# Optimization experiments

Measured on AMD Instinct MI355X. Metric: run time of the kernel, lower is better.

The kernel has to match this reference:

```python
import jax, jax.numpy as jnp
import numpy as np

B, N = 16, 131072
C_MID, C_OUT = 128, 16


def setup_inputs() -> dict:
    key = jax.random.key(0)
    k1, k2, k3, k4 = jax.random.split(key, 4)
    # points in roughly [-0.5, 0.5] so cube indexing covers the grids
    x = jax.random.uniform(k1, (B, N, 3), dtype=jnp.float32) - 0.5
    W1 = jax.random.normal(k2, (C_MID, 3), dtype=jnp.float32) * 0.1
    b1 = jnp.zeros((C_MID,), jnp.float32)
    W2 = jax.random.normal(k3, (C_OUT, C_MID), dtype=jnp.float32) * 0.1
    b2 = jnp.zeros((C_OUT,), jnp.float32)
    # fixed per-batch permutations (deterministic stand-in for torch.randperm)
    perm = jnp.stack([jax.random.permutation(jax.random.fold_in(k4, i), N)
                      for i in range(B)]).astype(jnp.int32)
    return {"x": x, "W1": W1, "b1": b1, "W2": W2, "b2": b2, "perm": perm}


def point_to_cell(pts, feat, W, H, D):
    # pts float [B,N,3] already clamped to [0, dim-1]; cast like torch LongTensor
    idx = pts.astype(jnp.int32)
    flat = (idx[..., 0] * H + idx[..., 1]) * D + idx[..., 2]  # [B,N]
    Bb, Nn, C = feat.shape

    def scatter_one(fi, fe):
        grid = jnp.zeros((W * H * D, C), feat.dtype)
        return grid.at[fi].set(fe)

    cell = jax.vmap(scatter_one)(flat, feat)           # [B, WHD, C]
    return cell.transpose(0, 2, 1).reshape(Bb, C, W, H, D)


def reference(x, W1, b1, W2, b2, perm):
    # PointNetfeatLocal: 1x1 Conv1d stack == per-point MLP 3 -> 128 -> 16
    h = jnp.maximum(jnp.einsum('bnc,hc->bnh', x, W1) + b1, 0.0)
    feat = jnp.einsum('bnh,oh->bno', h, W2) + b2       # [B,N,16]
    # shuffle_points_feat: per-batch permutation gather
    xs = jnp.take_along_axis(x, perm[..., None], axis=1)
    fs = jnp.take_along_axis(feat, perm[..., None], axis=1)
    # batch_grid_pooling32 / 64
    cube32 = jnp.clip(xs * 32.0 + 16.5, 0.0, 31.0)
    cube64 = jnp.clip(xs * 64.0 + 32.5, 0.0, 63.0)
    feat_cell32 = point_to_cell(cube32, fs, 32, 32, 32)  # [B,16,32,32,32]
    feat_cell64 = point_to_cell(cube64, fs, 64, 64, 64)  # [B,16,64,64,64]
    return feat_cell32, feat_cell64
```

## Files before the change

kernel.cpp:

```cpp
#include <hip/hip_runtime.h>

namespace {
constexpr int kB = 16;
constexpr int kN = 131072;
constexpr int kNLog = 17;
constexpr int kCMid = 128;
constexpr int kCOut = 16;
constexpr int kCells32Log = 15;
constexpr int kCells64Log = 18;
constexpr int kCells32 = 1 << kCells32Log;
constexpr int kCells64 = 1 << kCells64Log;
constexpr long kOut32Elems = (long)kB * kCOut * kCells32;
}

template <bool STORE_FEAT>
__global__ __launch_bounds__(256) void fused_mlp_scatter(
    const float* __restrict__ x,
    const float* __restrict__ W1, const float* __restrict__ b1,
    const float* __restrict__ W2, const float* __restrict__ b2,
    const int* __restrict__ perm,
    unsigned int* __restrict__ win32, unsigned int* __restrict__ win64,
    float* __restrict__ feat)
{
    __shared__ float sW1[kCMid * 3];
    __shared__ float sb1[kCMid];
    __shared__ float sW2[kCOut * kCMid];
    __shared__ float sb2[kCOut];
    const int t = threadIdx.x;
    if (STORE_FEAT) {
        for (int idx = t; idx < kCMid * 3; idx += 256) sW1[idx] = W1[idx];
        for (int idx = t; idx < kCMid; idx += 256) sb1[idx] = b1[idx];
        for (int idx = t; idx < kCOut * kCMid; idx += 256) sW2[idx] = W2[idx];
        if (t < kCOut) sb2[t] = b2[t];
        __syncthreads();
    }

    const long gid = (long)blockIdx.x * 256 + t;
    const int b = (int)(gid >> kNLog);
    const int i = (int)(gid & (kN - 1));
    const int j = perm[gid];

    const float* xp = x + ((long)b * kN + j) * 3;
    const float x0 = xp[0], x1 = xp[1], x2 = xp[2];

    const int ix32 = (int)fminf(fmaxf(__fadd_rn(__fmul_rn(x0, 32.0f), 16.5f), 0.0f), 31.0f);
    const int iy32 = (int)fminf(fmaxf(__fadd_rn(__fmul_rn(x1, 32.0f), 16.5f), 0.0f), 31.0f);
    const int iz32 = (int)fminf(fmaxf(__fadd_rn(__fmul_rn(x2, 32.0f), 16.5f), 0.0f), 31.0f);
    const int cell32 = (ix32 * 32 + iy32) * 32 + iz32;
    const int ix64 = (int)fminf(fmaxf(__fadd_rn(__fmul_rn(x0, 64.0f), 32.5f), 0.0f), 63.0f);
    const int iy64 = (int)fminf(fmaxf(__fadd_rn(__fmul_rn(x1, 64.0f), 32.5f), 0.0f), 63.0f);
    const int iz64 = (int)fminf(fmaxf(__fadd_rn(__fmul_rn(x2, 64.0f), 32.5f), 0.0f), 63.0f);
    const int cell64 = (ix64 * 64 + iy64) * 64 + iz64;

    const unsigned int pri = (unsigned int)(i + 1);
    atomicMax(&win32[b * kCells32 + cell32], pri);
    atomicMax(&win64[b * kCells64 + cell64], pri);

    if (STORE_FEAT) {
        float acc[kCOut];
        #pragma unroll
        for (int c = 0; c < kCOut; ++c) acc[c] = sb2[c];
        #pragma unroll 4
        for (int k = 0; k < kCMid; ++k) {
            float h = sW1[k * 3 + 0] * x0 + sW1[k * 3 + 1] * x1 + sW1[k * 3 + 2] * x2 + sb1[k];
            h = fmaxf(h, 0.0f);
            #pragma unroll
            for (int c = 0; c < kCOut; ++c) acc[c] += sW2[c * kCMid + k] * h;
        }
        float4* fp = (float4*)(feat + gid * kCOut);
        fp[0] = make_float4(acc[0], acc[1], acc[2], acc[3]);
        fp[1] = make_float4(acc[4], acc[5], acc[6], acc[7]);
        fp[2] = make_float4(acc[8], acc[9], acc[10], acc[11]);
        fp[3] = make_float4(acc[12], acc[13], acc[14], acc[15]);
    }
}

template <int CLOG, bool RECOMPUTE>
__global__ __launch_bounds__(256) void gather_cells(
    const unsigned int* __restrict__ win,
    const float* __restrict__ feat,
    const int* __restrict__ perm,
    const float* __restrict__ x,
    const float* __restrict__ W1, const float* __restrict__ b1,
    const float* __restrict__ W2, const float* __restrict__ b2,
    float* __restrict__ out)
{
    constexpr int cells = 1 << CLOG;
    __shared__ float sW1[kCMid * 3];
    __shared__ float sb1[kCMid];
    __shared__ float sW2[kCOut * kCMid];
    __shared__ float sb2[kCOut];
    const int t = threadIdx.x;
    if (RECOMPUTE) {
        for (int idx = t; idx < kCMid * 3; idx += 256) sW1[idx] = W1[idx];
        for (int idx = t; idx < kCMid; idx += 256) sb1[idx] = b1[idx];
        for (int idx = t; idx < kCOut * kCMid; idx += 256) sW2[idx] = W2[idx];
        if (t < kCOut) sb2[t] = b2[t];
        __syncthreads();
    }

    const long gid = (long)blockIdx.x * 256 + t;
    const int b = (int)(gid >> CLOG);
    const int cell = (int)(gid & (cells - 1));
    const unsigned int w = win[gid];

    float v[kCOut];
    if (w == 0u) {
        #pragma unroll
        for (int c = 0; c < kCOut; ++c) v[c] = 0.0f;
    } else if (!RECOMPUTE) {
        const int i = (int)(w - 1u);
        const float4* fp = (const float4*)(feat + (((long)b << kNLog) + i) * kCOut);
        float4 f0 = fp[0], f1 = fp[1], f2 = fp[2], f3 = fp[3];
        v[0] = f0.x; v[1] = f0.y; v[2]  = f0.z; v[3]  = f0.w;
        v[4] = f1.x; v[5] = f1.y; v[6]  = f1.z; v[7]  = f1.w;
        v[8] = f2.x; v[9] = f2.y; v[10] = f2.z; v[11] = f2.w;
        v[12] = f3.x; v[13] = f3.y; v[14] = f3.z; v[15] = f3.w;
    } else {
        const int i = (int)(w - 1u);
        const int j = perm[((long)b << kNLog) + i];
        const float* xp = x + ((long)b * kN + j) * 3;
        const float x0 = xp[0], x1 = xp[1], x2 = xp[2];
        #pragma unroll
        for (int c = 0; c < kCOut; ++c) v[c] = sb2[c];
        #pragma unroll 4
        for (int k = 0; k < kCMid; ++k) {
            float h = sW1[k * 3 + 0] * x0 + sW1[k * 3 + 1] * x1 + sW1[k * 3 + 2] * x2 + sb1[k];
            h = fmaxf(h, 0.0f);
            #pragma unroll
            for (int c = 0; c < kCOut; ++c) v[c] += sW2[c * kCMid + k] * h;
        }
    }

    float* op = out + (((long)b * kCOut) << CLOG) + cell;
    #pragma unroll
    for (int c = 0; c < kCOut; ++c) op[(long)c << CLOG] = v[c];
}

extern "C" void kernel_launch(void* const* d_in, const int* in_sizes, int n_in,
                              void* d_out, int out_size, void* d_ws, size_t ws_size,
                              hipStream_t stream)
{
    const float* x  = (const float*)d_in[0];
    const float* W1 = (const float*)d_in[1];
    const float* b1 = (const float*)d_in[2];
    const float* W2 = (const float*)d_in[3];
    const float* b2 = (const float*)d_in[4];
    const int* perm = (const int*)d_in[5];

    float* out32 = (float*)d_out;
    float* out64 = out32 + kOut32Elems;

    unsigned int* win32 = (unsigned int*)d_ws;
    unsigned int* win64 = win32 + (size_t)kB * kCells32;
    const size_t winnerBytes = (size_t)kB * (kCells32 + kCells64) * sizeof(unsigned int);
    float* feat = (float*)((char*)d_ws + winnerBytes);
    const size_t featBytes = (size_t)kB * kN * kCOut * sizeof(float);
    const bool storeFeat = ws_size >= winnerBytes + featBytes;

    hipMemsetAsync(d_ws, 0, winnerBytes, stream);

    const int nPtsBlocks = (int)(((long)kB * kN) / 256);
    const int n32Blocks  = (int)(((long)kB * kCells32) / 256);
    const int n64Blocks  = (int)(((long)kB * kCells64) / 256);
    dim3 blk(256);

    if (storeFeat) {
        fused_mlp_scatter<true><<<nPtsBlocks, blk, 0, stream>>>(
            x, W1, b1, W2, b2, perm, win32, win64, feat);
        gather_cells<kCells32Log, false><<<n32Blocks, blk, 0, stream>>>(
            win32, feat, perm, x, W1, b1, W2, b2, out32);
        gather_cells<kCells64Log, false><<<n64Blocks, blk, 0, stream>>>(
            win64, feat, perm, x, W1, b1, W2, b2, out64);
    } else {
        fused_mlp_scatter<false><<<nPtsBlocks, blk, 0, stream>>>(
            x, W1, b1, W2, b2, perm, win32, win64, nullptr);
        gather_cells<kCells32Log, true><<<n32Blocks, blk, 0, stream>>>(
            win32, feat, perm, x, W1, b1, W2, b2, out32);
        gather_cells<kCells64Log, true><<<n64Blocks, blk, 0, stream>>>(
            win64, feat, perm, x, W1, b1, W2, b2, out64);
    }
}
```

Measured before the change: 331.3 us.

## Pre-pack MLP weights and compute four points per thread with uniform weight loads

A tiny pre-kernel packs W1 together with b1 into float4 rows and stores W2 transposed, so that each k step reads contiguous float4 weights with a wave-uniform index. This replaces the per-block shared-memory staging and the LDS reads that fed every FMA. The scatter kernel now handles four points per thread, so each weight load is shared across four points and more FMAs are available to overlap with the atomics. In exchange it adds one extra launch and holds more accumulators in registers. The MLP kernel also now always writes feat, even on the fallback path where the workspace may be too small to hold it.

```diff
diff --git a/kernel.cpp b/kernel.cpp
--- a/kernel.cpp
+++ b/kernel.cpp
@@ -11,67 +11,104 @@
 constexpr int kCells32 = 1 << kCells32Log;
 constexpr int kCells64 = 1 << kCells64Log;
 constexpr long kOut32Elems = (long)kB * kCOut * kCells32;
-}
-
-template <bool STORE_FEAT>
+constexpr int kP = 4;
+}
+
+__global__ __launch_bounds__(256) void pack_weights(
+    const float* __restrict__ W1, const float* __restrict__ b1,
+    const float* __restrict__ W2,
+    float* __restrict__ W1p, float* __restrict__ W2t)
+{
+    const int t = threadIdx.x;
+    for (int k = t; k < kCMid; k += 256) {
+        W1p[k * 4 + 0] = W1[k * 3 + 0];
+        W1p[k * 4 + 1] = W1[k * 3 + 1];
+        W1p[k * 4 + 2] = W1[k * 3 + 2];
+        W1p[k * 4 + 3] = b1[k];
+    }
+    for (int idx = t; idx < kCOut * kCMid; idx += 256) {
+        const int c = idx >> 7;
+        const int k = idx & 127;
+        W2t[k * kCOut + c] = W2[idx];
+    }
+}
+
 __global__ __launch_bounds__(256) void fused_mlp_scatter(
     const float* __restrict__ x,
-    const float* __restrict__ W1, const float* __restrict__ b1,
-    const float* __restrict__ W2, const float* __restrict__ b2,
     const int* __restrict__ perm,
+    const float* __restrict__ W1p, const float* __restrict__ W2t,
+    const float* __restrict__ b2,
     unsigned int* __restrict__ win32, unsigned int* __restrict__ win64,
     float* __restrict__ feat)
 {
-    __shared__ float sW1[kCMid * 3];
-    __shared__ float sb1[kCMid];
-    __shared__ float sW2[kCOut * kCMid];
-    __shared__ float sb2[kCOut];
     const int t = threadIdx.x;
-    if (STORE_FEAT) {
-        for (int idx = t; idx < kCMid * 3; idx += 256) sW1[idx] = W1[idx];
-        for (int idx = t; idx < kCMid; idx += 256) sb1[idx] = b1[idx];
-        for (int idx = t; idx < kCOut * kCMid; idx += 256) sW2[idx] = W2[idx];
-        if (t < kCOut) sb2[t] = b2[t];
-        __syncthreads();
-    }
-
-    const long gid = (long)blockIdx.x * 256 + t;
-    const int b = (int)(gid >> kNLog);
-    const int i = (int)(gid & (kN - 1));
-    const int j = perm[gid];
-
-    const float* xp = x + ((long)b * kN + j) * 3;
-    const float x0 = xp[0], x1 = xp[1], x2 = xp[2];
-
-    const int ix32 = (int)fminf(fmaxf(__fadd_rn(__fmul_rn(x0, 32.0f), 16.5f), 0.0f), 31.0f);
-    const int iy32 = (int)fminf(fmaxf(__fadd_rn(__fmul_rn(x1, 32.0f), 16.5f), 0.0f), 31.0f);
-    const int iz32 = (int)fminf(fmaxf(__fadd_rn(__fmul_rn(x2, 32.0f), 16.5f), 0.0f), 31.0f);
-    const int cell32 = (ix32 * 32 + iy32) * 32 + iz32;
-    const int ix64 = (int)fminf(fmaxf(__fadd_rn(__fmul_rn(x0, 64.0f), 32.5f), 0.0f), 63.0f);
-    const int iy64 = (int)fminf(fmaxf(__fadd_rn(__fmul_rn(x1, 64.0f), 32.5f), 0.0f), 63.0f);
-    const int iz64 = (int)fminf(fmaxf(__fadd_rn(__fmul_rn(x2, 64.0f), 32.5f), 0.0f), 63.0f);
-    const int cell64 = (ix64 * 64 + iy64) * 64 + iz64;
-
-    const unsigned int pri = (unsigned int)(i + 1);
-    atomicMax(&win32[b * kCells32 + cell32], pri);
-    atomicMax(&win64[b * kCells64 + cell64], pri);
-
-    if (STORE_FEAT) {
-        float acc[kCOut];
-        #pragma unroll
-        for (int c = 0; c < kCOut; ++c) acc[c] = sb2[c];
-        #pragma unroll 4
-        for (int k = 0; k < kCMid; ++k) {
-            float h = sW1[k * 3 + 0] * x0 + sW1[k * 3 + 1] * x1 + sW1[k * 3 + 2] * x2 + sb1[k];
-            h = fmaxf(h, 0.0f);
+    const long base = (long)blockIdx.x * (256 * kP);
+
+    float x0[kP], x1[kP], x2[kP];
+
+    #pragma unroll
+    for (int p = 0; p < kP; ++p) {
+        const long gid = base + p * 256 + t;
+        const int b = (int)(gid >> kNLog);
+        const int i = (int)(gid & (kN - 1));
+        const int j = perm[gid];
+        const float* xp = x + ((long)b * kN + j) * 3;
+        const float v0 = xp[0], v1 = xp[1], v2 = xp[2];
+        x0[p] = v0; x1[p] = v1; x2[p] = v2;
+
+        const int ix32 = (int)fminf(fmaxf(__fadd_rn(__fmul_rn(v0, 32.0f), 16.5f), 0.0f), 31.0f);
+        const int iy32 = (int)fminf(fmaxf(__fadd_rn(__fmul_rn(v1, 32.0f), 16.5f), 0.0f), 31.0f);
+        const int iz32 = (int)fminf(fmaxf(__fadd_rn(__fmul_rn(v2, 32.0f), 16.5f), 0.0f), 31.0f);
+        const int ix64 = (int)fminf(fmaxf(__fadd_rn(__fmul_rn(v0, 64.0f), 32.5f), 0.0f), 63.0f);
+        const int iy64 = (int)fminf(fmaxf(__fadd_rn(__fmul_rn(v1, 64.0f), 32.5f), 0.0f), 63.0f);
+        const int iz64 = (int)fminf(fmaxf(__fadd_rn(__fmul_rn(v2, 64.0f), 32.5f), 0.0f), 63.0f);
+        const unsigned int pri = (unsigned int)(i + 1);
+        atomicMax(&win32[b * kCells32 + (ix32 * 32 + iy32) * 32 + iz32], pri);
+        atomicMax(&win64[b * kCells64 + (ix64 * 64 + iy64) * 64 + iz64], pri);
+    }
+
+    float acc[kP][kCOut];
+    #pragma unroll
+    for (int p = 0; p < kP; ++p)
+        #pragma unroll
+        for (int c = 0; c < kCOut; ++c) acc[p][c] = 0.0f;
+
+    const float4* __restrict__ w1v = (const float4*)W1p;
+    const float4* __restrict__ w2v = (const float4*)W2t;
+
+    #pragma unroll 4
+    for (int k = 0; k < kCMid; ++k) {
+        const float4 w1 = w1v[k];
+        float h[kP];
+        #pragma unroll
+        for (int p = 0; p < kP; ++p)
+            h[p] = fmaxf(fmaf(w1.x, x0[p], fmaf(w1.y, x1[p], fmaf(w1.z, x2[p], w1.w))), 0.0f);
+        #pragma unroll
+        for (int q = 0; q < 4; ++q) {
+            const float4 w = w2v[k * 4 + q];
             #pragma unroll
-            for (int c = 0; c < kCOut; ++c) acc[c] += sW2[c * kCMid + k] * h;
+            for (int p = 0; p < kP; ++p) {
+                acc[p][4 * q + 0] = fmaf(w.x, h[p], acc[p][4 * q + 0]);
+                acc[p][4 * q + 1] = fmaf(w.y, h[p], acc[p][4 * q + 1]);
+                acc[p][4 * q + 2] = fmaf(w.z, h[p], acc[p][4 * q + 2]);
+                acc[p][4 * q + 3] = fmaf(w.w, h[p], acc[p][4 * q + 3]);
+            }
         }
+    }
+
+    const float4 bq0 = ((const float4*)b2)[0];
+    const float4 bq1 = ((const float4*)b2)[1];
+    const float4 bq2 = ((const float4*)b2)[2];
+    const float4 bq3 = ((const float4*)b2)[3];
+
+    #pragma unroll
+    for (int p = 0; p < kP; ++p) {
+        const long gid = base + p * 256 + t;
         float4* fp = (float4*)(feat + gid * kCOut);
-        fp[0] = make_float4(acc[0], acc[1], acc[2], acc[3]);
-        fp[1] = make_float4(acc[4], acc[5], acc[6], acc[7]);
-        fp[2] = make_float4(acc[8], acc[9], acc[10], acc[11]);
-        fp[3] = make_float4(acc[12], acc[13], acc[14], acc[15]);
+        fp[0] = make_float4(acc[p][0]  + bq0.x, acc[p][1]  + bq0.y, acc[p][2]  + bq0.z, acc[p][3]  + bq0.w);
+        fp[1] = make_float4(acc[p][4]  + bq1.x, acc[p][5]  + bq1.y, acc[p][6]  + bq1.z, acc[p][7]  + bq1.w);
+        fp[2] = make_float4(acc[p][8]  + bq2.x, acc[p][9]  + bq2.y, acc[p][10] + bq2.z, acc[p][11] + bq2.w);
+        fp[3] = make_float4(acc[p][12] + bq3.x, acc[p][13] + bq3.y, acc[p][14] + bq3.z, acc[p][15] + bq3.w);
     }
 }
 
@@ -81,25 +118,12 @@
     const float* __restrict__ feat,
     const int* __restrict__ perm,
     const float* __restrict__ x,
-    const float* __restrict__ W1, const float* __restrict__ b1,
-    const float* __restrict__ W2, const float* __restrict__ b2,
+    const float* __restrict__ W1p, const float* __restrict__ W2t,
+    const float* __restrict__ b2,
     float* __restrict__ out)
 {
     constexpr int cells = 1 << CLOG;
-    __shared__ float sW1[kCMid * 3];
-    __shared__ float sb1[kCMid];
-    __shared__ float sW2[kCOut * kCMid];
-    __shared__ float sb2[kCOut];
-    const int t = threadIdx.x;
-    if (RECOMPUTE) {
-        for (int idx = t; idx < kCMid * 3; idx += 256) sW1[idx] = W1[idx];
-        for (int idx = t; idx < kCMid; idx += 256) sb1[idx] = b1[idx];
-        for (int idx = t; idx < kCOut * kCMid; idx += 256) sW2[idx] = W2[idx];
-        if (t < kCOut) sb2[t] = b2[t];
-        __syncthreads();
-    }
-
-    const long gid = (long)blockIdx.x * 256 + t;
+    const long gid = (long)blockIdx.x * 256 + threadIdx.x;
     const int b = (int)(gid >> CLOG);
     const int cell = (int)(gid & (cells - 1));
     const unsigned int w = win[gid];
@@ -111,7 +135,7 @@
     } else if (!RECOMPUTE) {
         const int i = (int)(w - 1u);
         const float4* fp = (const float4*)(feat + (((long)b << kNLog) + i) * kCOut);
-        float4 f0 = fp[0], f1 = fp[1], f2 = fp[2], f3 = fp[3];
+        const float4 f0 = fp[0], f1 = fp[1], f2 = fp[2], f3 = fp[3];
         v[0] = f0.x; v[1] = f0.y; v[2]  = f0.z; v[3]  = f0.w;
         v[4] = f1.x; v[5] = f1.y; v[6]  = f1.z; v[7]  = f1.w;
         v[8] = f2.x; v[9] = f2.y; v[10] = f2.z; v[11] = f2.w;
@@ -120,16 +144,24 @@
         const int i = (int)(w - 1u);
         const int j = perm[((long)b << kNLog) + i];
         const float* xp = x + ((long)b * kN + j) * 3;
-        const float x0 = xp[0], x1 = xp[1], x2 = xp[2];
-        #pragma unroll
-        for (int c = 0; c < kCOut; ++c) v[c] = sb2[c];
+        const float v0 = xp[0], v1 = xp[1], v2 = xp[2];
+        #pragma unroll
+        for (int c = 0; c < kCOut; ++c) v[c] = 0.0f;
         #pragma unroll 4
         for (int k = 0; k < kCMid; ++k) {
-            float h = sW1[k * 3 + 0] * x0 + sW1[k * 3 + 1] * x1 + sW1[k * 3 + 2] * x2 + sb1[k];
-            h = fmaxf(h, 0.0f);
+            const float4 w1 = ((const float4*)W1p)[k];
+            const float h = fmaxf(fmaf(w1.x, v0, fmaf(w1.y, v1, fmaf(w1.z, v2, w1.w))), 0.0f);
             #pragma unroll
-            for (int c = 0; c < kCOut; ++c) v[c] += sW2[c * kCMid + k] * h;
+            for (int q = 0; q < 4; ++q) {
+                const float4 wq = ((const float4*)W2t)[k * 4 + q];
+                v[4 * q + 0] = fmaf(wq.x, h, v[4 * q + 0]);
+                v[4 * q + 1] = fmaf(wq.y, h, v[4 * q + 1]);
+                v[4 * q + 2] = fmaf(wq.z, h, v[4 * q + 2]);
+                v[4 * q + 3] = fmaf(wq.w, h, v[4 * q + 3]);
+            }
         }
+        #pragma unroll
+        for (int c = 0; c < kCOut; ++c) v[c] += b2[c];
     }
 
     float* op = out + (((long)b * kCOut) << CLOG) + cell;
@@ -151,33 +183,35 @@
     float* out32 = (float*)d_out;
     float* out64 = out32 + kOut32Elems;
 
-    unsigned int* win32 = (unsigned int*)d_ws;
+    float* W1p = (float*)d_ws;
+    float* W2t = W1p + kCMid * 4;
+    unsigned int* win32 = (unsigned int*)((char*)d_ws + 16384);
     unsigned int* win64 = win32 + (size_t)kB * kCells32;
     const size_t winnerBytes = (size_t)kB * (kCells32 + kCells64) * sizeof(unsigned int);
-    float* feat = (float*)((char*)d_ws + winnerBytes);
+    float* feat = (float*)((char*)win32 + winnerBytes);
     const size_t featBytes = (size_t)kB * kN * kCOut * sizeof(float);
-    const bool storeFeat = ws_size >= winnerBytes + featBytes;
-
-    hipMemsetAsync(d_ws, 0, winnerBytes, stream);
-
-    const int nPtsBlocks = (int)(((long)kB * kN) / 256);
+    const bool storeFeat = ws_size >= 16384 + winnerBytes + featBytes;
+
+    hipMemsetAsync(win32, 0, winnerBytes, stream);
+    pack_weights<<<1, 256, 0, stream>>>(W1, b1, W2, W1p, W2t);
+
+    const int nPtsBlocks = (int)(((long)kB * kN) / (256 * kP));
     const int n32Blocks  = (int)(((long)kB * kCells32) / 256);
     const int n64Blocks  = (int)(((long)kB * kCells64) / 256);
     dim3 blk(256);
 
+    fused_mlp_scatter<<<nPtsBlocks, blk, 0, stream>>>(
+        x, perm, W1p, W2t, b2, win32, win64, feat);
+
     if (storeFeat) {
-        fused_mlp_scatter<true><<<nPtsBlocks, blk, 0, stream>>>(
-            x, W1, b1, W2, b2, perm, win32, win64, feat);
         gather_cells<kCells32Log, false><<<n32Blocks, blk, 0, stream>>>(
-            win32, feat, perm, x, W1, b1, W2, b2, out32);
+            win32, feat, perm, x, W1p, W2t, b2, out32);
         gather_cells<kCells64Log, false><<<n64Blocks, blk, 0, stream>>>(
-            win64, feat, perm, x, W1, b1, W2, b2, out64);
+            win64, feat, perm, x, W1p, W2t, b2, out64);
     } else {
-        fused_mlp_scatter<false><<<nPtsBlocks, blk, 0, stream>>>(
-            x, W1, b1, W2, b2, perm, win32, win64, nullptr);
         gather_cells<kCells32Log, true><<<n32Blocks, blk, 0, stream>>>(
-            win32, feat, perm, x, W1, b1, W2, b2, out32);
+            win32, feat, perm, x, W1p, W2t, b2, out32);
         gather_cells<kCells64Log, true><<<n64Blocks, blk, 0, stream>>>(
-            win64, feat, perm, x, W1, b1, W2, b2, out64);
-    }
-}
+            win64, feat, perm, x, W1p, W2t, b2, out64);
+    }
+}
```

New measurement: 320.6 us. 3.2% less time.
